# Optimization experiments

Hardware: AMD Instinct MI355X
Metric: run time of the kernel (lower is better)

## Reference

```python
import jax, jax.numpy as jnp
import numpy as np

CUTOFF = 5.0
LOG2 = 0.6931471805599453

def ssp(x):
    # ShiftedSoftplus: softplus(x) - log(2)
    return jax.nn.softplus(x) - LOG2

def setup_inputs() -> dict:
    key = jax.random.key(0)
    ks = jax.random.split(key, 10)
    B, P, A, G, F, E = 2, 4096, 96, 1, 32, 20
    return {
        "scalar": jax.random.normal(ks[0], (B, A, G, F), jnp.float32),
        "scalar_reciever": jax.random.normal(ks[1], (B, P, G, F), jnp.float32),
        "expansion": jax.random.uniform(ks[2], (B, P, A, E), jnp.float32),
        "mask": jax.random.uniform(ks[3], (B, P, A, G), jnp.float32),
        "edge_distance": jax.random.uniform(ks[4], (B, P, A, 1), jnp.float32) * CUTOFF,
        "W1e": jax.random.normal(ks[5], (E, F), jnp.float32) * 0.1,
        "b1e": jnp.zeros((F,), jnp.float32),
        "W2e": jax.random.normal(ks[6], (F, F), jnp.float32) * 0.1,
        "b2e": jnp.zeros((F,), jnp.float32),
        "W1n": jax.random.normal(ks[7], (2 * F, F), jnp.float32) * 0.1,
        "b1n": jnp.zeros((F,), jnp.float32),
        "W2n": jax.random.normal(ks[8], (F, F), jnp.float32) * 0.1,
        "b2n": jnp.zeros((F,), jnp.float32),
    }

def reference(scalar, scalar_reciever, expansion, mask, edge_distance,
              W1e, b1e, W2e, b2e, W1n, b1n, W2n, b2n):
    F = scalar.shape[-1]
    # edge gate: 2-layer MLP on expansion, times soft cutoff  -> [B,P,A,F]
    gates = ssp(expansion @ W1e + b1e) @ W2e + b2e
    gates = gates * (1.0 - jax.nn.sigmoid(5.0 * (edge_distance - (CUTOFF - 1.5))))
    # pairwise node MLP: split first linear into source/target halves instead of
    # materializing the [B,P,A,G,2F] repeat+concat tensor (same math).
    Ws, Wt = W1n[:F], W1n[F:]
    src = jnp.einsum('bagf,fh->bagh', scalar, Ws)            # [B,A,G,H]
    tgt = jnp.einsum('bpgf,fh->bpgh', scalar_reciever, Wt)   # [B,P,G,H]
    h = src[:, None, :, :, :] + tgt[:, :, None, :, :] + b1n  # [B,P,A,G,H]
    nodes = ssp(h) @ W2n + b2n                               # [B,P,A,G,F]
    result = mask[..., None] * (gates[..., None, :] * nodes)
    return jnp.sum(result, axis=-3)                          # sum over atoms A -> [B,P,G,F]

if __name__ == "__main__":
    out = reference(**setup_inputs())
    print(out.shape)
```

## Files before the change

### kernel.cpp

```cpp
#include <hip/hip_runtime.h>

#define NB   2
#define NP   4096
#define NA   96
#define NF   32
#define NE   20
#define NBP  (NB*NP)

typedef __attribute__((ext_vector_type(8)))  short bf16x8;
typedef __attribute__((ext_vector_type(16))) float f32x16;

union Frag { bf16x8 v; int i[4]; };

__device__ __forceinline__ int cvtpk(float lo, float hi) {
  int r;
  asm("v_cvt_pk_bf16_f32 %0, %1, %2" : "=v"(r) : "v"(lo), "v"(hi));
  return r;
}
__device__ __forceinline__ float ssp_f(float x) {
  float t = __expf(-fabsf(x));
  return fmaxf(x, 0.0f) + __logf(1.0f + t) - 0.69314718056f;
}
__device__ __forceinline__ f32x16 mfma32(const Frag a, const Frag b, f32x16 c) {
  return __builtin_amdgcn_mfma_f32_32x32x16_bf16(a.v, b.v, c, 0, 0, 0);
}
__device__ __forceinline__ f32x16 ld_bias16(const float* base ) {
  const float4* p = reinterpret_cast<const float4*>(base);
  float4 q0 = p[0], q1 = p[2], q2 = p[4], q3 = p[6];
  f32x16 c;
  c[0]=q0.x;  c[1]=q0.y;  c[2]=q0.z;  c[3]=q0.w;
  c[4]=q1.x;  c[5]=q1.y;  c[6]=q1.z;  c[7]=q1.w;
  c[8]=q2.x;  c[9]=q2.y;  c[10]=q2.z; c[11]=q2.w;
  c[12]=q3.x; c[13]=q3.y; c[14]=q3.z; c[15]=q3.w;
  return c;
}

__global__ __launch_bounds__(256)
void prep_kernel(const float* __restrict__ scalar,
                 const float* __restrict__ sr,
                 const float* __restrict__ W1n,
                 const float* __restrict__ b1n,
                 float* __restrict__ tgt_out,
                 float* __restrict__ src_ws)
{
  int i = blockIdx.x * 256 + threadIdx.x;
  int f   = i & 31;
  int row = i >> 5;
  const float* x;
  const float* W;
  float acc;
  if (row < NBP) { x = sr + row * NF;            W = W1n + NF * NF; acc = 0.0f;   }
  else           { x = scalar + (row - NBP) * NF; W = W1n;          acc = b1n[f]; }
  float4 xv[8];
#pragma unroll
  for (int q = 0; q < 8; ++q) xv[q] = reinterpret_cast<const float4*>(x)[q];
#pragma unroll
  for (int q = 0; q < 8; ++q) {
    acc = fmaf(xv[q].x, W[(4 * q + 0) * NF + f], acc);
    acc = fmaf(xv[q].y, W[(4 * q + 1) * NF + f], acc);
    acc = fmaf(xv[q].z, W[(4 * q + 2) * NF + f], acc);
    acc = fmaf(xv[q].w, W[(4 * q + 3) * NF + f], acc);
  }
  if (row < NBP) tgt_out[i] = acc;
  else           src_ws[(row - NBP) * NF + f] = acc;
}

__global__ __launch_bounds__(256, 3)
void fused_main(const float* __restrict__ expansion,
                const float* __restrict__ mask,
                const float* __restrict__ edge_dist,
                const float* __restrict__ W1e,
                const float* __restrict__ b1e,
                const float* __restrict__ W2e,
                const float* __restrict__ b2e,
                const float* __restrict__ W2n,
                const float* __restrict__ b2n,
                const float* __restrict__ src_ws,
                float* __restrict__ out)
{
  const int tid  = threadIdx.x;
  const int wid  = tid >> 6;
  const int lane = tid & 63;
  const int col  = lane & 31;
  const int hw   = lane >> 5;

  __shared__ __align__(16) float smb[96];
  if (tid < 32) {
    smb[tid]      = b1e[tid];
    smb[32 + tid] = b2e[tid];
    smb[64 + tid] = b2n[tid];
  }
  __syncthreads();
  const float* biasA = smb      + 4 * hw;
  const float* biasB = smb + 32 + 4 * hw;
  const float* biasC = smb + 64 + 4 * hw;

  Frag a1s0, a1s1, a2s0, a2s1, a3s0, a3s1;
#pragma unroll
  for (int r = 0; r < 4; ++r) {
    const int k0 = 8 * hw + 2 * r;
    const int k1 = 16 + k0;
    a1s0.i[r] = cvtpk(W1e[k0 * NF + col], W1e[(k0 + 1) * NF + col]);
    {
      float lo = (k1     < NE) ? W1e[k1 * NF + col]       : 0.0f;
      float hi = (k1 + 1 < NE) ? W1e[(k1 + 1) * NF + col] : 0.0f;
      a1s1.i[r] = cvtpk(lo, hi);
    }
    a2s0.i[r] = cvtpk(W2e[k0 * NF + col], W2e[(k0 + 1) * NF + col]);
    a2s1.i[r] = cvtpk(W2e[k1 * NF + col], W2e[(k1 + 1) * NF + col]);
    a3s0.i[r] = cvtpk(W2n[k0 * NF + col], W2n[(k0 + 1) * NF + col]);
    a3s1.i[r] = cvtpk(W2n[k1 * NF + col], W2n[(k1 + 1) * NF + col]);
  }

#pragma unroll 1
  for (int pi = 0; pi < 2; ++pi) {
    const int bp = blockIdx.x * 8 + wid * 2 + pi;
    const int b  = bp >> 12;

    const float* tg = out + bp * NF;
    float4 t0 = *reinterpret_cast<const float4*>(tg + 8 * hw);
    float4 t1 = *reinterpret_cast<const float4*>(tg + 8 * hw + 4);
    float4 t2 = *reinterpret_cast<const float4*>(tg + 16 + 8 * hw);
    float4 t3 = *reinterpret_cast<const float4*>(tg + 16 + 8 * hw + 4);

    const float* expb  = expansion + (size_t)bp * (NA * NE);
    const float* maskb = mask      + bp * NA;
    const float* distb = edge_dist + bp * NA;
    const float* srcb  = src_ws    + b * (NA * NF);

    float4 ef[3][3];
    float  mk[3], dd[3];
#pragma unroll
    for (int t = 0; t < 3; ++t) {
      const int a = t * 32 + col;
      const float* ea = expb + a * NE;
      ef[t][0] = *reinterpret_cast<const float4*>(ea + 8 * hw);
      ef[t][1] = *reinterpret_cast<const float4*>(ea + 8 * hw + 4);
      ef[t][2] = *reinterpret_cast<const float4*>(ea + 16);
      mk[t] = maskb[a];
      dd[t] = distb[a];
    }
    float em[3];
#pragma unroll
    for (int t = 0; t < 3; ++t) {
      const float z = __expf(5.0f * (dd[t] - 3.5f));
      em[t] = mk[t] * __builtin_amdgcn_rcpf(1.0f + z);
    }

    f32x16 acc;
#pragma unroll
    for (int r = 0; r < 16; ++r) acc[r] = 0.0f;

#pragma unroll
    for (int t = 0; t < 3; ++t) {
      const int a = t * 32 + col;

      Frag b1f0, b1f1;
      b1f0.i[0] = cvtpk(ef[t][0].x, ef[t][0].y);
      b1f0.i[1] = cvtpk(ef[t][0].z, ef[t][0].w);
      b1f0.i[2] = cvtpk(ef[t][1].x, ef[t][1].y);
      b1f0.i[3] = cvtpk(ef[t][1].z, ef[t][1].w);
      b1f1.i[0] = hw ? 0 : cvtpk(ef[t][2].x, ef[t][2].y);
      b1f1.i[1] = hw ? 0 : cvtpk(ef[t][2].z, ef[t][2].w);
      b1f1.i[2] = 0;
      b1f1.i[3] = 0;

      f32x16 d1 = ld_bias16(biasA);
      d1 = mfma32(a1s0, b1f0, d1);
      d1 = mfma32(a1s1, b1f1, d1);
#pragma unroll
      for (int r = 0; r < 16; ++r) d1[r] = ssp_f(d1[r]);

      int u0 = cvtpk(d1[0],  d1[1]);
      int u1 = cvtpk(d1[2],  d1[3]);
      int u2 = cvtpk(d1[4],  d1[5]);
      int u3 = cvtpk(d1[6],  d1[7]);
      int u4 = cvtpk(d1[8],  d1[9]);
      int u5 = cvtpk(d1[10], d1[11]);
      int u6 = cvtpk(d1[12], d1[13]);
      int u7 = cvtpk(d1[14], d1[15]);
      asm("v_permlane32_swap_b32 %0, %1" : "+v"(u0), "+v"(u2));
      asm("v_permlane32_swap_b32 %0, %1" : "+v"(u1), "+v"(u3));
      asm("v_permlane32_swap_b32 %0, %1" : "+v"(u4), "+v"(u6));
      asm("v_permlane32_swap_b32 %0, %1" : "+v"(u5), "+v"(u7));
      Frag b2f0, b2f1;
      b2f0.i[0] = u0; b2f0.i[1] = u1; b2f0.i[2] = u2; b2f0.i[3] = u3;
      b2f1.i[0] = u4; b2f1.i[1] = u5; b2f1.i[2] = u6; b2f1.i[3] = u7;

      f32x16 d2 = ld_bias16(biasB);
      d2 = mfma32(a2s0, b2f0, d2);
      d2 = mfma32(a2s1, b2f1, d2);

      const float* sa = srcb + a * NF;
      float4 s0 = *reinterpret_cast<const float4*>(sa + 8 * hw);
      float4 s1 = *reinterpret_cast<const float4*>(sa + 8 * hw + 4);
      float4 s2 = *reinterpret_cast<const float4*>(sa + 16 + 8 * hw);
      float4 s3 = *reinterpret_cast<const float4*>(sa + 16 + 8 * hw + 4);
      Frag b3f0, b3f1;
      b3f0.i[0] = cvtpk(ssp_f(s0.x + t0.x), ssp_f(s0.y + t0.y));
      b3f0.i[1] = cvtpk(ssp_f(s0.z + t0.z), ssp_f(s0.w + t0.w));
      b3f0.i[2] = cvtpk(ssp_f(s1.x + t1.x), ssp_f(s1.y + t1.y));
      b3f0.i[3] = cvtpk(ssp_f(s1.z + t1.z), ssp_f(s1.w + t1.w));
      b3f1.i[0] = cvtpk(ssp_f(s2.x + t2.x), ssp_f(s2.y + t2.y));
      b3f1.i[1] = cvtpk(ssp_f(s2.z + t2.z), ssp_f(s2.w + t2.w));
      b3f1.i[2] = cvtpk(ssp_f(s3.x + t3.x), ssp_f(s3.y + t3.y));
      b3f1.i[3] = cvtpk(ssp_f(s3.z + t3.z), ssp_f(s3.w + t3.w));

      f32x16 d3 = ld_bias16(biasC);
      d3 = mfma32(a3s0, b3f0, d3);
      d3 = mfma32(a3s1, b3f1, d3);

#pragma unroll
      for (int r = 0; r < 16; ++r) acc[r] = fmaf(em[t] * d2[r], d3[r], acc[r]);
    }

#pragma unroll
    for (int m = 1; m <= 16; m <<= 1) {
#pragma unroll
      for (int r = 0; r < 16; ++r) acc[r] += __shfl_xor(acc[r], m, 64);
    }

    if (col == 0) {
      float4* o = reinterpret_cast<float4*>(out + bp * NF);
#pragma unroll
      for (int q = 0; q < 4; ++q) {
        float4 v;
        v.x = acc[4 * q];     v.y = acc[4 * q + 1];
        v.z = acc[4 * q + 2]; v.w = acc[4 * q + 3];
        o[2 * q + hw] = v;
      }
    }
  }
}

extern "C" void kernel_launch(void* const* d_in, const int* in_sizes, int n_in,
                              void* d_out, int out_size, void* d_ws, size_t ws_size,
                              hipStream_t stream) {
  const float* scalar    = (const float*)d_in[0];
  const float* sreciever = (const float*)d_in[1];
  const float* expansion = (const float*)d_in[2];
  const float* maskp     = (const float*)d_in[3];
  const float* edist     = (const float*)d_in[4];
  const float* W1e       = (const float*)d_in[5];
  const float* b1e       = (const float*)d_in[6];
  const float* W2e       = (const float*)d_in[7];
  const float* b2e       = (const float*)d_in[8];
  const float* W1n       = (const float*)d_in[9];
  const float* b1n       = (const float*)d_in[10];
  const float* W2n       = (const float*)d_in[11];
  const float* b2n       = (const float*)d_in[12];
  float* out    = (float*)d_out;
  float* src_ws = (float*)d_ws;

  prep_kernel<<<1048, 256, 0, stream>>>(scalar, sreciever, W1n, b1n, out, src_ws);
  fused_main<<<NBP / 8, 256, 0, stream>>>(expansion, maskp, edist,
                                          W1e, b1e, W2e, b2e, W2n, b2n,
                                          src_ws, out);
}
```

Baseline: 149.8 us.

## Precompute bf16 weight fragments in prep kernel and use one wave per receiver

The prep kernel gains two extra blocks that convert W1e, W2e and W2n into packed bf16 MFMA A-fragments and store them in a workspace table. The main kernel now loads these fragments with six int4 loads per lane instead of doing many scalar loads and conversions. It also drops the two-iteration per-wave loop, so each wave handles one receiver and the grid doubles. The occupancy hint goes from 3 to 4 blocks. This cuts per-block prologue work and exposes more parallelism, at the cost of more blocks each paying the bias-load and sync setup.

```diff
diff --git a/kernel.cpp b/kernel.cpp
--- a/kernel.cpp
+++ b/kernel.cpp
@@ -38,44 +38,71 @@
 __global__ __launch_bounds__(256)
 void prep_kernel(const float* __restrict__ scalar,
                  const float* __restrict__ sr,
+                 const float* __restrict__ W1e,
+                 const float* __restrict__ W2e,
+                 const float* __restrict__ W2n,
                  const float* __restrict__ W1n,
                  const float* __restrict__ b1n,
                  float* __restrict__ tgt_out,
-                 float* __restrict__ src_ws)
+                 float* __restrict__ src_ws,
+                 int4* __restrict__ ftab)
 {
-  int i = blockIdx.x * 256 + threadIdx.x;
-  int f   = i & 31;
-  int row = i >> 5;
-  const float* x;
-  const float* W;
-  float acc;
-  if (row < NBP) { x = sr + row * NF;            W = W1n + NF * NF; acc = 0.0f;   }
-  else           { x = scalar + (row - NBP) * NF; W = W1n;          acc = b1n[f]; }
-  float4 xv[8];
-#pragma unroll
-  for (int q = 0; q < 8; ++q) xv[q] = reinterpret_cast<const float4*>(x)[q];
-#pragma unroll
-  for (int q = 0; q < 8; ++q) {
-    acc = fmaf(xv[q].x, W[(4 * q + 0) * NF + f], acc);
-    acc = fmaf(xv[q].y, W[(4 * q + 1) * NF + f], acc);
-    acc = fmaf(xv[q].z, W[(4 * q + 2) * NF + f], acc);
-    acc = fmaf(xv[q].w, W[(4 * q + 3) * NF + f], acc);
-  }
-  if (row < NBP) tgt_out[i] = acc;
-  else           src_ws[(row - NBP) * NF + f] = acc;
-}
-
-__global__ __launch_bounds__(256, 3)
+  const int blk = blockIdx.x;
+  if (blk < 1048) {
+    int i = blk * 256 + threadIdx.x;
+    int f   = i & 31;
+    int row = i >> 5;
+    const float* x;
+    const float* W;
+    float acc;
+    if (row < NBP) { x = sr + row * NF;             W = W1n + NF * NF; acc = 0.0f;   }
+    else           { x = scalar + (row - NBP) * NF; W = W1n;           acc = b1n[f]; }
+    float4 xv[8];
+#pragma unroll
+    for (int q = 0; q < 8; ++q) xv[q] = reinterpret_cast<const float4*>(x)[q];
+#pragma unroll
+    for (int q = 0; q < 8; ++q) {
+      acc = fmaf(xv[q].x, W[(4 * q + 0) * NF + f], acc);
+      acc = fmaf(xv[q].y, W[(4 * q + 1) * NF + f], acc);
+      acc = fmaf(xv[q].z, W[(4 * q + 2) * NF + f], acc);
+      acc = fmaf(xv[q].w, W[(4 * q + 3) * NF + f], acc);
+    }
+    if (row < NBP) tgt_out[i] = acc;
+    else           src_ws[(row - NBP) * NF + f] = acc;
+  } else {
+    int e = (blk - 1048) * 256 + threadIdx.x;
+    if (e < 384) {
+      const int f  = e >> 6;
+      const int l  = e & 63;
+      const int c  = l & 31;
+      const int hw = l >> 5;
+      const float* W = (f < 2) ? W1e : ((f < 4) ? W2e : W2n);
+      const int kbase = (f & 1) ? (16 + 8 * hw) : (8 * hw);
+      int4 v;
+      int* vi = reinterpret_cast<int*>(&v);
+#pragma unroll
+      for (int r = 0; r < 4; ++r) {
+        int ka = kbase + 2 * r, kb = ka + 1;
+        bool pa = (f == 1) && (ka >= NE);
+        bool pb = (f == 1) && (kb >= NE);
+        float lo = W[(pa ? 0 : ka) * NF + c]; lo = pa ? 0.0f : lo;
+        float hi = W[(pb ? 0 : kb) * NF + c]; hi = pb ? 0.0f : hi;
+        vi[r] = cvtpk(lo, hi);
+      }
+      ftab[e] = v;
+    }
+  }
+}
+
+__global__ __launch_bounds__(256, 4)
 void fused_main(const float* __restrict__ expansion,
                 const float* __restrict__ mask,
                 const float* __restrict__ edge_dist,
-                const float* __restrict__ W1e,
                 const float* __restrict__ b1e,
-                const float* __restrict__ W2e,
                 const float* __restrict__ b2e,
-                const float* __restrict__ W2n,
                 const float* __restrict__ b2n,
                 const float* __restrict__ src_ws,
+                const int4* __restrict__ ftab,
                 float* __restrict__ out)
 {
   const int tid  = threadIdx.x;
@@ -96,139 +123,135 @@
   const float* biasC = smb + 64 + 4 * hw;
 
   Frag a1s0, a1s1, a2s0, a2s1, a3s0, a3s1;
-#pragma unroll
-  for (int r = 0; r < 4; ++r) {
-    const int k0 = 8 * hw + 2 * r;
-    const int k1 = 16 + k0;
-    a1s0.i[r] = cvtpk(W1e[k0 * NF + col], W1e[(k0 + 1) * NF + col]);
-    {
-      float lo = (k1     < NE) ? W1e[k1 * NF + col]       : 0.0f;
-      float hi = (k1 + 1 < NE) ? W1e[(k1 + 1) * NF + col] : 0.0f;
-      a1s1.i[r] = cvtpk(lo, hi);
-    }
-    a2s0.i[r] = cvtpk(W2e[k0 * NF + col], W2e[(k0 + 1) * NF + col]);
-    a2s1.i[r] = cvtpk(W2e[k1 * NF + col], W2e[(k1 + 1) * NF + col]);
-    a3s0.i[r] = cvtpk(W2n[k0 * NF + col], W2n[(k0 + 1) * NF + col]);
-    a3s1.i[r] = cvtpk(W2n[k1 * NF + col], W2n[(k1 + 1) * NF + col]);
-  }
-
-#pragma unroll 1
-  for (int pi = 0; pi < 2; ++pi) {
-    const int bp = blockIdx.x * 8 + wid * 2 + pi;
-    const int b  = bp >> 12;
-
-    const float* tg = out + bp * NF;
-    float4 t0 = *reinterpret_cast<const float4*>(tg + 8 * hw);
-    float4 t1 = *reinterpret_cast<const float4*>(tg + 8 * hw + 4);
-    float4 t2 = *reinterpret_cast<const float4*>(tg + 16 + 8 * hw);
-    float4 t3 = *reinterpret_cast<const float4*>(tg + 16 + 8 * hw + 4);
-
-    const float* expb  = expansion + (size_t)bp * (NA * NE);
-    const float* maskb = mask      + bp * NA;
-    const float* distb = edge_dist + bp * NA;
-    const float* srcb  = src_ws    + b * (NA * NF);
-
-    float4 ef[3][3];
-    float  mk[3], dd[3];
-#pragma unroll
-    for (int t = 0; t < 3; ++t) {
-      const int a = t * 32 + col;
-      const float* ea = expb + a * NE;
-      ef[t][0] = *reinterpret_cast<const float4*>(ea + 8 * hw);
-      ef[t][1] = *reinterpret_cast<const float4*>(ea + 8 * hw + 4);
-      ef[t][2] = *reinterpret_cast<const float4*>(ea + 16);
-      mk[t] = maskb[a];
-      dd[t] = distb[a];
-    }
-    float em[3];
-#pragma unroll
-    for (int t = 0; t < 3; ++t) {
-      const float z = __expf(5.0f * (dd[t] - 3.5f));
-      em[t] = mk[t] * __builtin_amdgcn_rcpf(1.0f + z);
-    }
-
-    f32x16 acc;
-#pragma unroll
-    for (int r = 0; r < 16; ++r) acc[r] = 0.0f;
-
-#pragma unroll
-    for (int t = 0; t < 3; ++t) {
-      const int a = t * 32 + col;
-
-      Frag b1f0, b1f1;
-      b1f0.i[0] = cvtpk(ef[t][0].x, ef[t][0].y);
-      b1f0.i[1] = cvtpk(ef[t][0].z, ef[t][0].w);
-      b1f0.i[2] = cvtpk(ef[t][1].x, ef[t][1].y);
-      b1f0.i[3] = cvtpk(ef[t][1].z, ef[t][1].w);
-      b1f1.i[0] = hw ? 0 : cvtpk(ef[t][2].x, ef[t][2].y);
-      b1f1.i[1] = hw ? 0 : cvtpk(ef[t][2].z, ef[t][2].w);
-      b1f1.i[2] = 0;
-      b1f1.i[3] = 0;
-
-      f32x16 d1 = ld_bias16(biasA);
-      d1 = mfma32(a1s0, b1f0, d1);
-      d1 = mfma32(a1s1, b1f1, d1);
-#pragma unroll
-      for (int r = 0; r < 16; ++r) d1[r] = ssp_f(d1[r]);
-
-      int u0 = cvtpk(d1[0],  d1[1]);
-      int u1 = cvtpk(d1[2],  d1[3]);
-      int u2 = cvtpk(d1[4],  d1[5]);
-      int u3 = cvtpk(d1[6],  d1[7]);
-      int u4 = cvtpk(d1[8],  d1[9]);
-      int u5 = cvtpk(d1[10], d1[11]);
-      int u6 = cvtpk(d1[12], d1[13]);
-      int u7 = cvtpk(d1[14], d1[15]);
-      asm("v_permlane32_swap_b32 %0, %1" : "+v"(u0), "+v"(u2));
-      asm("v_permlane32_swap_b32 %0, %1" : "+v"(u1), "+v"(u3));
-      asm("v_permlane32_swap_b32 %0, %1" : "+v"(u4), "+v"(u6));
-      asm("v_permlane32_swap_b32 %0, %1" : "+v"(u5), "+v"(u7));
-      Frag b2f0, b2f1;
-      b2f0.i[0] = u0; b2f0.i[1] = u1; b2f0.i[2] = u2; b2f0.i[3] = u3;
-      b2f1.i[0] = u4; b2f1.i[1] = u5; b2f1.i[2] = u6; b2f1.i[3] = u7;
-
-      f32x16 d2 = ld_bias16(biasB);
-      d2 = mfma32(a2s0, b2f0, d2);
-      d2 = mfma32(a2s1, b2f1, d2);
-
-      const float* sa = srcb + a * NF;
-      float4 s0 = *reinterpret_cast<const float4*>(sa + 8 * hw);
-      float4 s1 = *reinterpret_cast<const float4*>(sa + 8 * hw + 4);
-      float4 s2 = *reinterpret_cast<const float4*>(sa + 16 + 8 * hw);
-      float4 s3 = *reinterpret_cast<const float4*>(sa + 16 + 8 * hw + 4);
-      Frag b3f0, b3f1;
-      b3f0.i[0] = cvtpk(ssp_f(s0.x + t0.x), ssp_f(s0.y + t0.y));
-      b3f0.i[1] = cvtpk(ssp_f(s0.z + t0.z), ssp_f(s0.w + t0.w));
-      b3f0.i[2] = cvtpk(ssp_f(s1.x + t1.x), ssp_f(s1.y + t1.y));
-      b3f0.i[3] = cvtpk(ssp_f(s1.z + t1.z), ssp_f(s1.w + t1.w));
-      b3f1.i[0] = cvtpk(ssp_f(s2.x + t2.x), ssp_f(s2.y + t2.y));
-      b3f1.i[1] = cvtpk(ssp_f(s2.z + t2.z), ssp_f(s2.w + t2.w));
-      b3f1.i[2] = cvtpk(ssp_f(s3.x + t3.x), ssp_f(s3.y + t3.y));
-      b3f1.i[3] = cvtpk(ssp_f(s3.z + t3.z), ssp_f(s3.w + t3.w));
-
-      f32x16 d3 = ld_bias16(biasC);
-      d3 = mfma32(a3s0, b3f0, d3);
-      d3 = mfma32(a3s1, b3f1, d3);
-
-#pragma unroll
-      for (int r = 0; r < 16; ++r) acc[r] = fmaf(em[t] * d2[r], d3[r], acc[r]);
-    }
-
-#pragma unroll
-    for (int m = 1; m <= 16; m <<= 1) {
-#pragma unroll
-      for (int r = 0; r < 16; ++r) acc[r] += __shfl_xor(acc[r], m, 64);
-    }
-
-    if (col == 0) {
-      float4* o = reinterpret_cast<float4*>(out + bp * NF);
-#pragma unroll
-      for (int q = 0; q < 4; ++q) {
-        float4 v;
-        v.x = acc[4 * q];     v.y = acc[4 * q + 1];
-        v.z = acc[4 * q + 2]; v.w = acc[4 * q + 3];
-        o[2 * q + hw] = v;
-      }
+  {
+    int4 w0 = ftab[0 * 64 + lane];
+    int4 w1 = ftab[1 * 64 + lane];
+    int4 w2 = ftab[2 * 64 + lane];
+    int4 w3 = ftab[3 * 64 + lane];
+    int4 w4 = ftab[4 * 64 + lane];
+    int4 w5 = ftab[5 * 64 + lane];
+    a1s0.i[0]=w0.x; a1s0.i[1]=w0.y; a1s0.i[2]=w0.z; a1s0.i[3]=w0.w;
+    a1s1.i[0]=w1.x; a1s1.i[1]=w1.y; a1s1.i[2]=w1.z; a1s1.i[3]=w1.w;
+    a2s0.i[0]=w2.x; a2s0.i[1]=w2.y; a2s0.i[2]=w2.z; a2s0.i[3]=w2.w;
+    a2s1.i[0]=w3.x; a2s1.i[1]=w3.y; a2s1.i[2]=w3.z; a2s1.i[3]=w3.w;
+    a3s0.i[0]=w4.x; a3s0.i[1]=w4.y; a3s0.i[2]=w4.z; a3s0.i[3]=w4.w;
+    a3s1.i[0]=w5.x; a3s1.i[1]=w5.y; a3s1.i[2]=w5.z; a3s1.i[3]=w5.w;
+  }
+
+  const int bp = blockIdx.x * 4 + wid;
+  const int b  = bp >> 12;
+
+  const float* tg = out + bp * NF;
+  float4 t0 = *reinterpret_cast<const float4*>(tg + 8 * hw);
+  float4 t1 = *reinterpret_cast<const float4*>(tg + 8 * hw + 4);
+  float4 t2 = *reinterpret_cast<const float4*>(tg + 16 + 8 * hw);
+  float4 t3 = *reinterpret_cast<const float4*>(tg + 16 + 8 * hw + 4);
+
+  const float* expb  = expansion + (size_t)bp * (NA * NE);
+  const float* maskb = mask      + bp * NA;
+  const float* distb = edge_dist + bp * NA;
+  const float* srcb  = src_ws    + b * (NA * NF);
+
+  float4 ef[3][3];
+  float  mk[3], dd[3];
+#pragma unroll
+  for (int t = 0; t < 3; ++t) {
+    const int a = t * 32 + col;
+    const float* ea = expb + a * NE;
+    ef[t][0] = *reinterpret_cast<const float4*>(ea + 8 * hw);
+    ef[t][1] = *reinterpret_cast<const float4*>(ea + 8 * hw + 4);
+    ef[t][2] = *reinterpret_cast<const float4*>(ea + 16);
+    mk[t] = maskb[a];
+    dd[t] = distb[a];
+  }
+  float em[3];
+#pragma unroll
+  for (int t = 0; t < 3; ++t) {
+    const float z = __expf(5.0f * (dd[t] - 3.5f));
+    em[t] = mk[t] * __builtin_amdgcn_rcpf(1.0f + z);
+  }
+
+  f32x16 acc;
+#pragma unroll
+  for (int r = 0; r < 16; ++r) acc[r] = 0.0f;
+
+#pragma unroll
+  for (int t = 0; t < 3; ++t) {
+    const int a = t * 32 + col;
+
+    Frag b1f0, b1f1;
+    b1f0.i[0] = cvtpk(ef[t][0].x, ef[t][0].y);
+    b1f0.i[1] = cvtpk(ef[t][0].z, ef[t][0].w);
+    b1f0.i[2] = cvtpk(ef[t][1].x, ef[t][1].y);
+    b1f0.i[3] = cvtpk(ef[t][1].z, ef[t][1].w);
+    b1f1.i[0] = hw ? 0 : cvtpk(ef[t][2].x, ef[t][2].y);
+    b1f1.i[1] = hw ? 0 : cvtpk(ef[t][2].z, ef[t][2].w);
+    b1f1.i[2] = 0;
+    b1f1.i[3] = 0;
+
+    f32x16 d1 = ld_bias16(biasA);
+    d1 = mfma32(a1s0, b1f0, d1);
+    d1 = mfma32(a1s1, b1f1, d1);
+#pragma unroll
+    for (int r = 0; r < 16; ++r) d1[r] = ssp_f(d1[r]);
+
+    int u0 = cvtpk(d1[0],  d1[1]);
+    int u1 = cvtpk(d1[2],  d1[3]);
+    int u2 = cvtpk(d1[4],  d1[5]);
+    int u3 = cvtpk(d1[6],  d1[7]);
+    int u4 = cvtpk(d1[8],  d1[9]);
+    int u5 = cvtpk(d1[10], d1[11]);
+    int u6 = cvtpk(d1[12], d1[13]);
+    int u7 = cvtpk(d1[14], d1[15]);
+    asm("v_permlane32_swap_b32 %0, %1" : "+v"(u0), "+v"(u2));
+    asm("v_permlane32_swap_b32 %0, %1" : "+v"(u1), "+v"(u3));
+    asm("v_permlane32_swap_b32 %0, %1" : "+v"(u4), "+v"(u6));
+    asm("v_permlane32_swap_b32 %0, %1" : "+v"(u5), "+v"(u7));
+    Frag b2f0, b2f1;
+    b2f0.i[0] = u0; b2f0.i[1] = u1; b2f0.i[2] = u2; b2f0.i[3] = u3;
+    b2f1.i[0] = u4; b2f1.i[1] = u5; b2f1.i[2] = u6; b2f1.i[3] = u7;
+
+    f32x16 d2 = ld_bias16(biasB);
+    d2 = mfma32(a2s0, b2f0, d2);
+    d2 = mfma32(a2s1, b2f1, d2);
+
+    const float* sa = srcb + a * NF;
+    float4 s0 = *reinterpret_cast<const float4*>(sa + 8 * hw);
+    float4 s1 = *reinterpret_cast<const float4*>(sa + 8 * hw + 4);
+    float4 s2 = *reinterpret_cast<const float4*>(sa + 16 + 8 * hw);
+    float4 s3 = *reinterpret_cast<const float4*>(sa + 16 + 8 * hw + 4);
+    Frag b3f0, b3f1;
+    b3f0.i[0] = cvtpk(ssp_f(s0.x + t0.x), ssp_f(s0.y + t0.y));
+    b3f0.i[1] = cvtpk(ssp_f(s0.z + t0.z), ssp_f(s0.w + t0.w));
+    b3f0.i[2] = cvtpk(ssp_f(s1.x + t1.x), ssp_f(s1.y + t1.y));
+    b3f0.i[3] = cvtpk(ssp_f(s1.z + t1.z), ssp_f(s1.w + t1.w));
+    b3f1.i[0] = cvtpk(ssp_f(s2.x + t2.x), ssp_f(s2.y + t2.y));
+    b3f1.i[1] = cvtpk(ssp_f(s2.z + t2.z), ssp_f(s2.w + t2.w));
+    b3f1.i[2] = cvtpk(ssp_f(s3.x + t3.x), ssp_f(s3.y + t3.y));
+    b3f1.i[3] = cvtpk(ssp_f(s3.z + t3.z), ssp_f(s3.w + t3.w));
+
+    f32x16 d3 = ld_bias16(biasC);
+    d3 = mfma32(a3s0, b3f0, d3);
+    d3 = mfma32(a3s1, b3f1, d3);
+
+#pragma unroll
+    for (int r = 0; r < 16; ++r) acc[r] = fmaf(em[t] * d2[r], d3[r], acc[r]);
+  }
+
+#pragma unroll
+  for (int m = 1; m <= 16; m <<= 1) {
+#pragma unroll
+    for (int r = 0; r < 16; ++r) acc[r] += __shfl_xor(acc[r], m, 64);
+  }
+
+  if (col == 0) {
+    float4* o = reinterpret_cast<float4*>(out + bp * NF);
+#pragma unroll
+    for (int q = 0; q < 4; ++q) {
+      float4 v;
+      v.x = acc[4 * q];     v.y = acc[4 * q + 1];
+      v.z = acc[4 * q + 2]; v.w = acc[4 * q + 3];
+      o[2 * q + hw] = v;
     }
   }
 }
@@ -251,9 +274,10 @@
   const float* b2n       = (const float*)d_in[12];
   float* out    = (float*)d_out;
   float* src_ws = (float*)d_ws;
-
-  prep_kernel<<<1048, 256, 0, stream>>>(scalar, sreciever, W1n, b1n, out, src_ws);
-  fused_main<<<NBP / 8, 256, 0, stream>>>(expansion, maskp, edist,
-                                          W1e, b1e, W2e, b2e, W2n, b2n,
-                                          src_ws, out);
-}
+  int4*  ftab   = (int4*)((char*)d_ws + 192 * NF * 4);
+
+  prep_kernel<<<1050, 256, 0, stream>>>(scalar, sreciever, W1e, W2e, W2n,
+                                        W1n, b1n, out, src_ws, ftab);
+  fused_main<<<NBP / 4, 256, 0, stream>>>(expansion, maskp, edist,
+                                          b1e, b2e, b2n, src_ws, ftab, out);
+}
```

New measurement: 158.6 us. +5.9%, slower.
